# Performance work log

Measured on AMD Instinct MI355X. Metric: run time of the kernel, lower is better.

The kernel has to match this reference:

```python
import jax, jax.numpy as jnp
import numpy as np

N = 50000        # nodes
E = 600000       # edges
D = 128          # hidden dim
FID = 128        # fixed_input_dim (one-hot size)
RWSE = 16        # rwse_dim
G = 128          # num graphs
L = 4            # num GIN blocks
DEG = 1001       # degree embedding table (clamp to 1000)
GIN_EPS = 0.0
BN_EPS = 1e-5


def setup_inputs() -> dict:
    key = jax.random.key(0)
    ks = jax.random.split(key, 16)
    s = 0.05
    inp = {
        "feat_id": jax.random.randint(ks[0], (N,), 0, 100000),
        "edge_index": jax.random.randint(ks[1], (2, E), 0, N),
        "batch_idx": jnp.sort(jax.random.randint(ks[2], (N,), 0, G)),
        "rwse": jax.random.normal(ks[3], (N, RWSE), jnp.float32),
        "in_degrees": jax.random.randint(ks[4], (N,), 0, DEG),
        # parameters
        "value_W": jax.random.normal(ks[5], (FID, D), jnp.float32) * s,
        "value_b": jnp.zeros((D,), jnp.float32),
        "rwse_W": jax.random.normal(ks[6], (RWSE, D), jnp.float32) * s,
        "rwse_b": jnp.zeros((D,), jnp.float32),
        "deg_emb": jax.random.normal(ks[7], (DEG, D), jnp.float32) * s,
        "mlp_W1": jax.random.normal(ks[8], (L, D, D), jnp.float32) * s,
        "mlp_b1": jnp.zeros((L, D), jnp.float32),
        "mlp_W2": jax.random.normal(ks[9], (L, D, D), jnp.float32) * s,
        "mlp_b2": jnp.zeros((L, D), jnp.float32),
        "bn_gamma": 1.0 + jax.random.normal(ks[10], (L, D), jnp.float32) * s,
        "bn_beta": jax.random.normal(ks[11], (L, D), jnp.float32) * s,
        "bn_mean": jax.random.normal(ks[12], (L, D), jnp.float32) * s,
        "bn_var": 1.0 + jax.random.uniform(ks[13], (L, D), jnp.float32) * 0.1,
    }
    return inp


def reference(feat_id, edge_index, batch_idx, rwse, in_degrees,
              value_W, value_b, rwse_W, rwse_b, deg_emb,
              mlp_W1, mlp_b1, mlp_W2, mlp_b2,
              bn_gamma, bn_beta, bn_mean, bn_var):
    # one_hot(feat_id % FID) @ value_W  ==  row gather of value_W
    h_id = jnp.remainder(feat_id, FID)
    h_attr = value_W[h_id] + value_b                      # [N, D]
    h_attr = h_attr + rwse @ rwse_W + rwse_b              # rwse projection
    deg = jnp.clip(in_degrees, 0, DEG - 1)
    h = h_attr + deg_emb[deg]                             # [N, D]

    src, dst = edge_index[0], edge_index[1]
    for l in range(L):
        # GIN aggregation: sum of neighbor messages + (1+eps)*self
        agg = jax.ops.segment_sum(h[src], dst, num_segments=N)
        agg = agg + (1.0 + GIN_EPS) * h
        # MLP: Linear -> ReLU -> Linear
        m = jax.nn.relu(agg @ mlp_W1[l] + mlp_b1[l]) @ mlp_W2[l] + mlp_b2[l]
        # BatchNorm (inference stats) + ReLU
        inv = bn_gamma[l] * jax.lax.rsqrt(bn_var[l] + BN_EPS)
        h = jax.nn.relu((m - bn_mean[l]) * inv + bn_beta[l])

    # scatter-mean graph pooling
    pooled = jax.ops.segment_sum(h, batch_idx, num_segments=G)      # [G, D]
    count = jax.ops.segment_sum(jnp.ones((N, 1), h.dtype), batch_idx,
                                num_segments=G)                     # [G, 1]
    graph_feature = pooled / jnp.maximum(count, 1.0)
    return graph_feature, h
```

## Files before the change

### kernel.cpp

```cpp
#include <hip/hip_runtime.h>

#define N_NODES 50000
#define N_EDGES 600000
#define DIM 128
#define NGRAPH 128
#define NLAYER 4
#define BN_EPS 1e-5f
#define SCAN_BLK 1024

#define EN_BLOCKS 3125
#define WT_BLOCKS 512
#define HB_BLOCKS 2344

using short8  = __attribute__((ext_vector_type(8))) short;
using float4v = __attribute__((ext_vector_type(4))) float;

__device__ __forceinline__ float bf2f(unsigned short u) {
    union { unsigned int i; float f; } c; c.i = ((unsigned int)u) << 16; return c.f;
}
__device__ __forceinline__ unsigned short f2bf(float f) {
    union { float f; unsigned int i; } c; c.f = f;
    unsigned int x = c.i;
    return (unsigned short)((x + 0x7fffu + ((x >> 16) & 1u)) >> 16);
}

__global__ void fused_pre_kernel(const int* __restrict__ feat_id,
                                 const float* __restrict__ rwse,
                                 const int* __restrict__ indeg,
                                 const float* __restrict__ value_W,
                                 const float* __restrict__ value_b,
                                 const float* __restrict__ rwse_W,
                                 const float* __restrict__ rwse_b,
                                 const float* __restrict__ deg_emb,
                                 unsigned short* __restrict__ hout,
                                 const float* __restrict__ W1,
                                 const float* __restrict__ W2,
                                 unsigned short* __restrict__ w1t,
                                 unsigned short* __restrict__ w2t,
                                 const int* __restrict__ dst,
                                 int* __restrict__ cnt)
{
    int b = blockIdx.x;
    if (b < EN_BLOCKS) {
        __shared__ float srw[16][16];
        __shared__ int   sfid[16], sdeg[16];
        const int t = threadIdx.x;
        const int base = b * 16;
        srw[t >> 4][t & 15] = rwse[(size_t)base * 16 + t];
        if (t < 16) sfid[t] = feat_id[base + t] & 127;
        else if (t < 32) {
            int dg = indeg[base + t - 16];
            sdeg[t - 16] = dg < 0 ? 0 : (dg > 1000 ? 1000 : dg);
        }
        const int d = t & 127, half = t >> 7;
        float wk[16];
#pragma unroll
        for (int k = 0; k < 16; ++k) wk[k] = rwse_W[k * DIM + d];
        float vb = value_b[d] + rwse_b[d];
        __syncthreads();
#pragma unroll
        for (int nn = 0; nn < 8; ++nn) {
            int nl = half * 8 + nn;
            int node = base + nl;
            float v = value_W[sfid[nl] * DIM + d] + vb + deg_emb[sdeg[nl] * DIM + d];
            float acc = 0.f;
#pragma unroll
            for (int k = 0; k < 16; ++k) acc += srw[nl][k] * wk[k];
            hout[(size_t)node * DIM + d] = f2bf(v + acc);
        }
    } else if (b < EN_BLOCKS + WT_BLOCKS) {
        int idx = (b - EN_BLOCKS) * 256 + threadIdx.x;
        int i = idx & (DIM * DIM - 1);
        int l = (idx >> 14) & 3;
        int is2 = idx >= NLAYER * DIM * DIM;
        int n = i >> 7, k = i & 127;
        const float* W = (is2 ? W2 : W1) + l * DIM * DIM;
        unsigned short v = f2bf(W[k * DIM + n]);
        (is2 ? w2t : w1t)[l * DIM * DIM + n * DIM + k] = v;
    } else {
        int e = (b - EN_BLOCKS - WT_BLOCKS) * 256 + threadIdx.x;
        if (e < N_EDGES) atomicAdd(&cnt[dst[e]], 1);
    }
}

__global__ void scanA_kernel(const int* __restrict__ cnt, int* __restrict__ rp, int* __restrict__ bsum) {
    __shared__ int sc[SCAN_BLK];
    int t = threadIdx.x, i = blockIdx.x * SCAN_BLK + t;
    int v = (i < N_NODES) ? cnt[i] : 0;
    sc[t] = v; __syncthreads();
    for (int off = 1; off < SCAN_BLK; off <<= 1) {
        int add = (t >= off) ? sc[t - off] : 0;
        __syncthreads();
        sc[t] += add;
        __syncthreads();
    }
    if (i < N_NODES) rp[i] = sc[t] - v;
    if (t == SCAN_BLK - 1) bsum[blockIdx.x] = sc[t];
}

__global__ void scan_fixup_kernel(int* __restrict__ rp, const int* __restrict__ bsum,
                                  int* __restrict__ cur, int nsb) {
    __shared__ int sbx[64];
    int t = threadIdx.x;
    if (t < 64) {
        int v = (t < nsb) ? bsum[t] : 0;
        int orig = v;
        for (int off = 1; off < 64; off <<= 1) {
            int y = __shfl_up(v, off, 64);
            if (t >= off) v += y;
        }
        sbx[t] = v - orig;
    }
    __syncthreads();
    int i = blockIdx.x * 256 + t;
    if (i < N_NODES) { int v = rp[i] + sbx[i >> 10]; rp[i] = v; cur[i] = v; }
    else if (i == N_NODES) rp[i] = N_EDGES;
}

__global__ void scatter_kernel(const int* __restrict__ src, const int* __restrict__ dst,
                               int* __restrict__ cur, int* __restrict__ esrc) {
    int e = blockIdx.x * blockDim.x + threadIdx.x;
    if (e < N_EDGES) {
        int pos = atomicAdd(&cur[dst[e]], 1);
        esrc[pos] = src[e];
    }
}

__global__ void __launch_bounds__(256, 8) layer_kernel(
    const unsigned short* __restrict__ hin,
    const int* __restrict__ rp,
    const int* __restrict__ esrc,
    const unsigned short* __restrict__ w1t,
    const unsigned short* __restrict__ w2t,
    const float* __restrict__ b1, const float* __restrict__ b2,
    const float* __restrict__ gam, const float* __restrict__ bet,
    const float* __restrict__ mean, const float* __restrict__ var,
    unsigned short* __restrict__ hout, float* __restrict__ fout, int last)
{
    __shared__ unsigned short sA[16 * DIM];
    __shared__ unsigned short sM[16 * DIM];
    __shared__ int sRp[17];
    const int tid = threadIdx.x;
    const int wave = tid >> 6, lane = tid & 63;
    const int fr = lane & 15, fg = lane >> 4;
    const int base = blockIdx.x * 16;

    if (tid < 17) sRp[tid] = rp[base + tid];

    const int selfrow = wave * 4 + fg;
    uint4 selfv = *(const uint4*)(hin + (size_t)(base + selfrow) * DIM + fr * 8);

    __syncthreads();

    int e_[4], e1_[4], sfirst_[4];
#pragma unroll
    for (int j = 0; j < 4; ++j) {
        int row = wave * 4 + j;
        e_[j]  = sRp[row] + fg;
        e1_[j] = sRp[row + 1];
        sfirst_[j] = (e_[j] < e1_[j]) ? esrc[e_[j]] : 0;
    }

#pragma unroll
    for (int j = 0; j < 4; ++j) {
        int row = wave * 4 + j;
        float a[8];
#pragma unroll
        for (int i = 0; i < 8; ++i) a[i] = 0.f;
        int e = e_[j], e1v = e1_[j];
        int snext = sfirst_[j];
        while (e < e1v) {
            int s = snext;
            int en = e + 4;
            snext = (en < e1v) ? esrc[en] : 0;
            uint4 v = *(const uint4*)(hin + (size_t)s * DIM + fr * 8);
            a[0] += bf2f((unsigned short)(v.x & 0xffff)); a[1] += bf2f((unsigned short)(v.x >> 16));
            a[2] += bf2f((unsigned short)(v.y & 0xffff)); a[3] += bf2f((unsigned short)(v.y >> 16));
            a[4] += bf2f((unsigned short)(v.z & 0xffff)); a[5] += bf2f((unsigned short)(v.z >> 16));
            a[6] += bf2f((unsigned short)(v.w & 0xffff)); a[7] += bf2f((unsigned short)(v.w >> 16));
            e = en;
        }
#pragma unroll
        for (int i = 0; i < 8; ++i) {
            a[i] += __shfl_xor(a[i], 16, 64);
            a[i] += __shfl_xor(a[i], 32, 64);
        }
        if (fg == j) {
            a[0] += bf2f((unsigned short)(selfv.x & 0xffff)); a[1] += bf2f((unsigned short)(selfv.x >> 16));
            a[2] += bf2f((unsigned short)(selfv.y & 0xffff)); a[3] += bf2f((unsigned short)(selfv.y >> 16));
            a[4] += bf2f((unsigned short)(selfv.z & 0xffff)); a[5] += bf2f((unsigned short)(selfv.z >> 16));
            a[6] += bf2f((unsigned short)(selfv.w & 0xffff)); a[7] += bf2f((unsigned short)(selfv.w >> 16));
            uint4 o;
            o.x = (unsigned int)f2bf(a[0]) | ((unsigned int)f2bf(a[1]) << 16);
            o.y = (unsigned int)f2bf(a[2]) | ((unsigned int)f2bf(a[3]) << 16);
            o.z = (unsigned int)f2bf(a[4]) | ((unsigned int)f2bf(a[5]) << 16);
            o.w = (unsigned int)f2bf(a[6]) | ((unsigned int)f2bf(a[7]) << 16);
            int byte = row * 256 + fr * 16; byte ^= (row & 7) << 4;
            *(uint4*)((char*)sA + byte) = o;
        }
    }
    __syncthreads();

    short8 a0, a1, a2, a3;
    {
        int sw = (fr & 7) << 4;
        a0 = *(const short8*)((char*)sA + ((fr * 256 + (0  + fg * 8) * 2) ^ sw));
        a1 = *(const short8*)((char*)sA + ((fr * 256 + (32 + fg * 8) * 2) ^ sw));
        a2 = *(const short8*)((char*)sA + ((fr * 256 + (64 + fg * 8) * 2) ^ sw));
        a3 = *(const short8*)((char*)sA + ((fr * 256 + (96 + fg * 8) * 2) ^ sw));
    }

    float4v acc[2];
    acc[0] = (float4v){0.f, 0.f, 0.f, 0.f};
    acc[1] = (float4v){0.f, 0.f, 0.f, 0.f};

    const unsigned short* bp1 = w1t + (wave * 32 + fr) * DIM + fg * 8;
#pragma unroll
    for (int nb = 0; nb < 2; ++nb) {
        const unsigned short* bb = bp1 + nb * 16 * DIM;
        short8 b0 = *(const short8*)(bb);
        short8 b1v = *(const short8*)(bb + 32);
        short8 b2v = *(const short8*)(bb + 64);
        short8 b3v = *(const short8*)(bb + 96);
        acc[nb] = __builtin_amdgcn_mfma_f32_16x16x32_bf16(a0, b0, acc[nb], 0, 0, 0);
        acc[nb] = __builtin_amdgcn_mfma_f32_16x16x32_bf16(a1, b1v, acc[nb], 0, 0, 0);
        acc[nb] = __builtin_amdgcn_mfma_f32_16x16x32_bf16(a2, b2v, acc[nb], 0, 0, 0);
        acc[nb] = __builtin_amdgcn_mfma_f32_16x16x32_bf16(a3, b3v, acc[nb], 0, 0, 0);
    }

#pragma unroll
    for (int nb = 0; nb < 2; ++nb) {
        int col = wave * 32 + nb * 16 + fr;
        float bias = b1[col];
#pragma unroll
        for (int r = 0; r < 4; ++r) {
            int row = fg * 4 + r;
            float v = acc[nb][r] + bias;
            v = fmaxf(v, 0.f);
            int byte = row * 256 + col * 2; byte ^= (row & 7) << 4;
            *(unsigned short*)((char*)sM + byte) = f2bf(v);
        }
    }
    __syncthreads();

    short8 m0, m1, m2, m3;
    {
        int sw = (fr & 7) << 4;
        m0 = *(const short8*)((char*)sM + ((fr * 256 + (0  + fg * 8) * 2) ^ sw));
        m1 = *(const short8*)((char*)sM + ((fr * 256 + (32 + fg * 8) * 2) ^ sw));
        m2 = *(const short8*)((char*)sM + ((fr * 256 + (64 + fg * 8) * 2) ^ sw));
        m3 = *(const short8*)((char*)sM + ((fr * 256 + (96 + fg * 8) * 2) ^ sw));
    }

    float4v acc2[2];
    acc2[0] = (float4v){0.f, 0.f, 0.f, 0.f};
    acc2[1] = (float4v){0.f, 0.f, 0.f, 0.f};

    const unsigned short* bp2 = w2t + (wave * 32 + fr) * DIM + fg * 8;
#pragma unroll
    for (int nb = 0; nb < 2; ++nb) {
        const unsigned short* bb = bp2 + nb * 16 * DIM;
        short8 b0 = *(const short8*)(bb);
        short8 b1v = *(const short8*)(bb + 32);
        short8 b2v = *(const short8*)(bb + 64);
        short8 b3v = *(const short8*)(bb + 96);
        acc2[nb] = __builtin_amdgcn_mfma_f32_16x16x32_bf16(m0, b0, acc2[nb], 0, 0, 0);
        acc2[nb] = __builtin_amdgcn_mfma_f32_16x16x32_bf16(m1, b1v, acc2[nb], 0, 0, 0);
        acc2[nb] = __builtin_amdgcn_mfma_f32_16x16x32_bf16(m2, b2v, acc2[nb], 0, 0, 0);
        acc2[nb] = __builtin_amdgcn_mfma_f32_16x16x32_bf16(m3, b3v, acc2[nb], 0, 0, 0);
    }

#pragma unroll
    for (int nb = 0; nb < 2; ++nb) {
        int col = wave * 32 + nb * 16 + fr;
        float bias = b2[col];
        float iv = gam[col] * rsqrtf(var[col] + BN_EPS);
        float mn = mean[col], bt = bet[col];
#pragma unroll
        for (int r = 0; r < 4; ++r) {
            int node = base + fg * 4 + r;
            float v = acc2[nb][r] + bias;
            v = (v - mn) * iv + bt;
            v = fmaxf(v, 0.f);
            if (last) fout[(size_t)node * DIM + col] = v;
            else hout[(size_t)node * DIM + col] = f2bf(v);
        }
    }
}

__global__ void __launch_bounds__(256) pool_partial_kernel(const float* __restrict__ h,
                                                           const int* __restrict__ batch,
                                                           float* __restrict__ partial)
{
    __shared__ float sums[256];
    __shared__ int sb[2];
    int g = blockIdx.x >> 3, split = blockIdx.x & 7;
    if (threadIdx.x < 2) {
        int target = g + threadIdx.x;
        int lo = 0, hi = N_NODES;
        while (lo < hi) { int mid = (lo + hi) >> 1; if (batch[mid] < target) lo = mid + 1; else hi = mid; }
        sb[threadIdx.x] = lo;
    }
    __syncthreads();
    int lo = sb[0], hi = sb[1];
    int d = threadIdx.x & 127, half = threadIdx.x >> 7;
    float acc = 0.f;
    for (int n = lo + split * 2 + half; n < hi; n += 16) acc += h[(size_t)n * DIM + d];
    sums[threadIdx.x] = acc;
    __syncthreads();
    if (threadIdx.x < 128)
        partial[blockIdx.x * DIM + threadIdx.x] = sums[threadIdx.x] + sums[threadIdx.x + 128];
}

__global__ void pool_comb_kernel(const float* __restrict__ partial,
                                 const int* __restrict__ batch,
                                 float* __restrict__ out)
{
    __shared__ int sb[2];
    int g = blockIdx.x, t = threadIdx.x;
    if (t < 2) {
        int target = g + t;
        int lo = 0, hi = N_NODES;
        while (lo < hi) { int mid = (lo + hi) >> 1; if (batch[mid] < target) lo = mid + 1; else hi = mid; }
        sb[t] = lo;
    }
    __syncthreads();
    float s = 0.f;
#pragma unroll
    for (int sp = 0; sp < 8; ++sp) s += partial[(g * 8 + sp) * DIM + t];
    float c = (float)(sb[1] - sb[0]);
    out[g * DIM + t] = s / fmaxf(c, 1.f);
}

extern "C" void kernel_launch(void* const* d_in, const int* in_sizes, int n_in,
                              void* d_out, int out_size, void* d_ws, size_t ws_size,
                              hipStream_t stream)
{
    const int*   feat_id = (const int*)d_in[0];
    const int*   eidx    = (const int*)d_in[1];
    const int*   batch   = (const int*)d_in[2];
    const float* rwse    = (const float*)d_in[3];
    const int*   indeg   = (const int*)d_in[4];
    const float* value_W = (const float*)d_in[5];
    const float* value_b = (const float*)d_in[6];
    const float* rwse_W  = (const float*)d_in[7];
    const float* rwse_b  = (const float*)d_in[8];
    const float* deg_emb = (const float*)d_in[9];
    const float* W1      = (const float*)d_in[10];
    const float* b1      = (const float*)d_in[11];
    const float* W2      = (const float*)d_in[12];
    const float* b2      = (const float*)d_in[13];
    const float* gam     = (const float*)d_in[14];
    const float* bet     = (const float*)d_in[15];
    const float* mean    = (const float*)d_in[16];
    const float* var     = (const float*)d_in[17];

    const int* srcv = eidx;
    const int* dstv = eidx + N_EDGES;

    char* p = (char*)d_ws;
    auto alloc = [&](size_t bytes) { char* r = p; p += (bytes + 255) & ~(size_t)255; return r; };
    unsigned short* hA   = (unsigned short*)alloc((size_t)N_NODES * DIM * 2);
    unsigned short* hB   = (unsigned short*)alloc((size_t)N_NODES * DIM * 2);
    int* cnt  = (int*)alloc((size_t)N_NODES * 4);
    int* rp   = (int*)alloc((size_t)(N_NODES + 1) * 4);
    int* cur  = (int*)alloc((size_t)N_NODES * 4);
    int* bsum = (int*)alloc(64 * 4);
    int* esrc = (int*)alloc((size_t)N_EDGES * 4);
    unsigned short* w1t = (unsigned short*)alloc((size_t)NLAYER * DIM * DIM * 2);
    unsigned short* w2t = (unsigned short*)alloc((size_t)NLAYER * DIM * DIM * 2);
    float* partial = (float*)alloc((size_t)NGRAPH * 8 * DIM * 4);

    float* out = (float*)d_out;
    float* hf  = out + NGRAPH * DIM;

    hipMemsetAsync(cnt, 0, (size_t)N_NODES * 4, stream);
    fused_pre_kernel<<<EN_BLOCKS + WT_BLOCKS + HB_BLOCKS, 256, 0, stream>>>(
        feat_id, rwse, indeg, value_W, value_b, rwse_W, rwse_b, deg_emb, hA,
        W1, W2, w1t, w2t, dstv, cnt);
    int nsb = (N_NODES + SCAN_BLK - 1) / SCAN_BLK;
    scanA_kernel<<<nsb, SCAN_BLK, 0, stream>>>(cnt, rp, bsum);
    scan_fixup_kernel<<<(N_NODES + 1 + 255) / 256, 256, 0, stream>>>(rp, bsum, cur, nsb);
    scatter_kernel<<<(N_EDGES + 255) / 256, 256, 0, stream>>>(srcv, dstv, cur, esrc);

    const int nlb = N_NODES / 16;
    for (int l = 0; l < NLAYER; ++l) {
        const unsigned short* hi = (l & 1) ? hB : hA;
        unsigned short*       ho = (l & 1) ? hA : hB;
        layer_kernel<<<nlb, 256, 0, stream>>>(hi, rp, esrc,
            w1t + l * DIM * DIM, w2t + l * DIM * DIM,
            b1 + l * DIM, b2 + l * DIM, gam + l * DIM, bet + l * DIM,
            mean + l * DIM, var + l * DIM,
            ho, hf, (l == NLAYER - 1) ? 1 : 0);
    }
    pool_partial_kernel<<<NGRAPH * 8, 256, 0, stream>>>(hf, batch, partial);
    pool_comb_kernel<<<NGRAPH, DIM, 0, stream>>>(partial, batch, out);
}
```

Baseline: 381.3 us.

## Fuse graph pooling sums into last GIN layer epilogue via atomics

The last layer kernel now accumulates per-graph column sums directly from its epilogue. It uses per-thread run-length partial sums over sorted batch indices, then float atomicAdd into the output buffer, which is zeroed by a memset beforehand. The separate pool_partial kernel, which re-read the full fp32 node features, is removed along with the partial buffer, and a small kernel divides by node counts. This saves a 25MB read and a launch, at the cost of many contended atomics and non-deterministic float summation order.

```diff
diff --git a/kernel.cpp b/kernel.cpp
--- a/kernel.cpp
+++ b/kernel.cpp
@@ -135,17 +135,20 @@
     const float* __restrict__ b1, const float* __restrict__ b2,
     const float* __restrict__ gam, const float* __restrict__ bet,
     const float* __restrict__ mean, const float* __restrict__ var,
-    unsigned short* __restrict__ hout, float* __restrict__ fout, int last)
+    unsigned short* __restrict__ hout, float* __restrict__ fout,
+    const int* __restrict__ batch, float* __restrict__ pool, int last)
 {
     __shared__ unsigned short sA[16 * DIM];
     __shared__ unsigned short sM[16 * DIM];
     __shared__ int sRp[17];
+    __shared__ int sBatch[16];
     const int tid = threadIdx.x;
     const int wave = tid >> 6, lane = tid & 63;
     const int fr = lane & 15, fg = lane >> 4;
     const int base = blockIdx.x * 16;
 
     if (tid < 17) sRp[tid] = rp[base + tid];
+    if (last && tid >= 32 && tid < 48) sBatch[tid - 32] = batch[base + tid - 32];
 
     const int selfrow = wave * 4 + fg;
     uint4 selfv = *(const uint4*)(hin + (size_t)(base + selfrow) * DIM + fr * 8);
@@ -276,25 +279,39 @@
         float bias = b2[col];
         float iv = gam[col] * rsqrtf(var[col] + BN_EPS);
         float mn = mean[col], bt = bet[col];
-#pragma unroll
-        for (int r = 0; r < 4; ++r) {
-            int node = base + fg * 4 + r;
-            float v = acc2[nb][r] + bias;
-            v = (v - mn) * iv + bt;
-            v = fmaxf(v, 0.f);
-            if (last) fout[(size_t)node * DIM + col] = v;
-            else hout[(size_t)node * DIM + col] = f2bf(v);
-        }
-    }
-}
-
-__global__ void __launch_bounds__(256) pool_partial_kernel(const float* __restrict__ h,
-                                                           const int* __restrict__ batch,
-                                                           float* __restrict__ partial)
+        if (last) {
+            float s = 0.f;
+            int g = sBatch[fg * 4];
+#pragma unroll
+            for (int r = 0; r < 4; ++r) {
+                int row = fg * 4 + r;
+                int node = base + row;
+                float v = acc2[nb][r] + bias;
+                v = (v - mn) * iv + bt;
+                v = fmaxf(v, 0.f);
+                fout[(size_t)node * DIM + col] = v;
+                int gr = sBatch[row];
+                if (gr != g) { atomicAdd(&pool[(size_t)g * DIM + col], s); s = 0.f; g = gr; }
+                s += v;
+            }
+            atomicAdd(&pool[(size_t)g * DIM + col], s);
+        } else {
+#pragma unroll
+            for (int r = 0; r < 4; ++r) {
+                int node = base + fg * 4 + r;
+                float v = acc2[nb][r] + bias;
+                v = (v - mn) * iv + bt;
+                v = fmaxf(v, 0.f);
+                hout[(size_t)node * DIM + col] = f2bf(v);
+            }
+        }
+    }
+}
+
+__global__ void pool_div_kernel(const int* __restrict__ batch, float* __restrict__ out)
 {
-    __shared__ float sums[256];
     __shared__ int sb[2];
-    int g = blockIdx.x >> 3, split = blockIdx.x & 7;
+    int g = blockIdx.x;
     if (threadIdx.x < 2) {
         int target = g + threadIdx.x;
         int lo = 0, hi = N_NODES;
@@ -302,34 +319,8 @@
         sb[threadIdx.x] = lo;
     }
     __syncthreads();
-    int lo = sb[0], hi = sb[1];
-    int d = threadIdx.x & 127, half = threadIdx.x >> 7;
-    float acc = 0.f;
-    for (int n = lo + split * 2 + half; n < hi; n += 16) acc += h[(size_t)n * DIM + d];
-    sums[threadIdx.x] = acc;
-    __syncthreads();
-    if (threadIdx.x < 128)
-        partial[blockIdx.x * DIM + threadIdx.x] = sums[threadIdx.x] + sums[threadIdx.x + 128];
-}
-
-__global__ void pool_comb_kernel(const float* __restrict__ partial,
-                                 const int* __restrict__ batch,
-                                 float* __restrict__ out)
-{
-    __shared__ int sb[2];
-    int g = blockIdx.x, t = threadIdx.x;
-    if (t < 2) {
-        int target = g + t;
-        int lo = 0, hi = N_NODES;
-        while (lo < hi) { int mid = (lo + hi) >> 1; if (batch[mid] < target) lo = mid + 1; else hi = mid; }
-        sb[t] = lo;
-    }
-    __syncthreads();
-    float s = 0.f;
-#pragma unroll
-    for (int sp = 0; sp < 8; ++sp) s += partial[(g * 8 + sp) * DIM + t];
     float c = (float)(sb[1] - sb[0]);
-    out[g * DIM + t] = s / fmaxf(c, 1.f);
+    out[g * DIM + threadIdx.x] /= fmaxf(c, 1.f);
 }
 
 extern "C" void kernel_launch(void* const* d_in, const int* in_sizes, int n_in,
@@ -369,12 +360,12 @@
     int* esrc = (int*)alloc((size_t)N_EDGES * 4);
     unsigned short* w1t = (unsigned short*)alloc((size_t)NLAYER * DIM * DIM * 2);
     unsigned short* w2t = (unsigned short*)alloc((size_t)NLAYER * DIM * DIM * 2);
-    float* partial = (float*)alloc((size_t)NGRAPH * 8 * DIM * 4);
 
     float* out = (float*)d_out;
     float* hf  = out + NGRAPH * DIM;
 
     hipMemsetAsync(cnt, 0, (size_t)N_NODES * 4, stream);
+    hipMemsetAsync(out, 0, (size_t)NGRAPH * DIM * 4, stream);
     fused_pre_kernel<<<EN_BLOCKS + WT_BLOCKS + HB_BLOCKS, 256, 0, stream>>>(
         feat_id, rwse, indeg, value_W, value_b, rwse_W, rwse_b, deg_emb, hA,
         W1, W2, w1t, w2t, dstv, cnt);
@@ -391,8 +382,7 @@
             w1t + l * DIM * DIM, w2t + l * DIM * DIM,
             b1 + l * DIM, b2 + l * DIM, gam + l * DIM, bet + l * DIM,
             mean + l * DIM, var + l * DIM,
-            ho, hf, (l == NLAYER - 1) ? 1 : 0);
-    }
-    pool_partial_kernel<<<NGRAPH * 8, 256, 0, stream>>>(hf, batch, partial);
-    pool_comb_kernel<<<NGRAPH, DIM, 0, stream>>>(partial, batch, out);
-}
+            ho, hf, batch, out, (l == NLAYER - 1) ? 1 : 0);
+    }
+    pool_div_kernel<<<NGRAPH, DIM, 0, stream>>>(batch, out);
+}
```

New measurement: 390.5 us. +2.4%, slower.
